# Optimization experiments

Hardware: AMD Instinct MI355X
Metric: run time of the kernel (lower is better)

Reference implementation:

```python
import jax, jax.numpy as jnp
import numpy as np
from jax import lax

NUM_CLASSES = 21
KSIZE = 11
DIL = 1
BLUR = 4
NUM_STEPS = 5
YX_SCALE = 80.0
RGB_SCALE = 13.0
POS_SCALE = 3.0


def _ceil_pad_factor(sizes, factor):
    offs = tuple((factor - s % factor) % factor for s in sizes)
    return tuple((o + 1) // 2 for o in offs)


def avg_pool_nopad(x, k, pad):
    # F.avg_pool2d(kernel=stride=k, padding=pad, count_include_pad=False)
    pcfg = ((0, 0), (0, 0), (pad[0], pad[0]), (pad[1], pad[1]))
    s = lax.reduce_window(x, jnp.float32(0), lax.add, (1, 1, k, k), (1, 1, k, k), pcfg)
    ones = jnp.ones((1, 1) + x.shape[2:], x.dtype)
    cnt = lax.reduce_window(ones, jnp.float32(0), lax.add, (1, 1, k, k), (1, 1, k, k), pcfg)
    return s / cnt


def _patches(x, k, dil):
    # im2col with zero padding (matches torch F.unfold used by pac)
    pad = (k // 2) * dil
    p = lax.conv_general_dilated_patches(
        x, (k, k), (1, 1), [(pad, pad), (pad, pad)], rhs_dilation=(dil, dil))
    B, C, H, W = x.shape
    return p.reshape(B, C, k * k, H, W)


def gaussian_kernel(feat, k, dil):
    # pixel-adaptive Gaussian kernel: exp(-0.5 * ||f_i - f_j||^2) over the KxK window
    p = _patches(feat, k, dil)                       # [B,F,k2,H,W]
    d = p - feat[:, :, None]
    return jnp.exp(-0.5 * jnp.sum(d * d, axis=1))    # [B,k2,H,W]


def pac_message(Q, kernel, k, dil):
    # shared-filter (Potts, spatial_filter=False) pac conv: per-channel kernel-weighted sum
    p = _patches(Q, k, dil)                          # [B,C,k2,h,w]
    return jnp.einsum('bckhw,bkhw->bchw', p, kernel)


def upsample_bilinear(x, scale):
    # matches F.interpolate(mode='bilinear', align_corners=False)
    B, C, h, w = x.shape
    def idx_w(n_in):
        n_out = n_in * scale
        src = jnp.clip((jnp.arange(n_out, dtype=jnp.float32) + 0.5) / scale - 0.5, 0.0, n_in - 1.0)
        i0 = jnp.floor(src).astype(jnp.int32)
        i1 = jnp.minimum(i0 + 1, n_in - 1)
        return i0, i1, (src - i0).astype(x.dtype)
    y0, y1, wy = idx_w(h)
    x0, x1, wx = idx_w(w)
    xh = x[:, :, y0, :] * (1 - wy)[None, None, :, None] + x[:, :, y1, :] * wy[None, None, :, None]
    return xh[:, :, :, x0] * (1 - wx)[None, None, None, :] + xh[:, :, :, x1] * wx[None, None, None, :]


def crf_forward(x, w_backbone, b_backbone, unary_weight, pairwise_weights):
    B, _, H, W = x.shape
    # backbone stub: 3x3 conv producing unary logits [B,21,H,W]
    unary = lax.conv_general_dilated(
        x, w_backbone, (1, 1), [(1, 1), (1, 1)],
        dimension_numbers=('NCHW', 'OIHW', 'NCHW')) + b_backbone[None, :, None, None]
    # edge features: bilateral (YX/80, RGB/13) and spatial (YX/3)
    yx = jnp.stack(jnp.meshgrid(jnp.arange(H, dtype=x.dtype), jnp.arange(W, dtype=x.dtype), indexing='ij'))
    yx = jnp.broadcast_to(yx[None], (B, 2, H, W))
    feat_bilateral = jnp.concatenate([yx / YX_SCALE, x / RGB_SCALE], axis=1)  # [B,5,H,W]
    feat_spatial = yx / POS_SCALE                                             # [B,2,H,W]
    pad = _ceil_pad_factor((H, W), BLUR)
    kernels = [gaussian_kernel(avg_pool_nopad(f, BLUR, pad), KSIZE, DIL)
               for f in (feat_bilateral, feat_spatial)]

    def step(logQ, unary, k1, k2, uw, pw):
        Q = jax.nn.softmax(logQ, axis=1)
        Qb = avg_pool_nopad(Q, BLUR, pad)
        new = uw * unary
        for kern, w in ((k1, pw[0]), (k2, pw[1])):
            msg = pac_message(Qb, kern, KSIZE, DIL)
            msg = upsample_bilinear(msg, BLUR)[:, :, pad[0]:pad[0] + H, pad[1]:pad[1] + W]
            new = new + w * msg
        return new

    logQ = unary
    for _ in range(NUM_STEPS):
        logQ = step(logQ, unary, kernels[0], kernels[1], unary_weight, pairwise_weights)
    return logQ  # final_output == 'log_Q'


def setup_inputs():
    key = jax.random.key(0)
    ks = jax.random.split(key, 3)
    B, H, W = 2, 512, 512
    x = jax.random.uniform(ks[0], (B, 3, H, W), jnp.float32) * 255.0  # image in [0,255]
    w_backbone = jax.random.normal(ks[1], (NUM_CLASSES, 3, 3, 3), jnp.float32) * 0.1
    b_backbone = jax.random.normal(ks[2], (NUM_CLASSES,), jnp.float32) * 0.01
    unary_weight = jnp.asarray(0.8, jnp.float32)
    pairwise_weights = jnp.asarray([2.0, 0.6], jnp.float32)
    return {"x": x, "w_backbone": w_backbone, "b_backbone": b_backbone,
            "unary_weight": unary_weight, "pairwise_weights": pairwise_weights}


def reference(x, w_backbone, b_backbone, unary_weight, pairwise_weights):
    return crf_forward(x, w_backbone, b_backbone, unary_weight, pairwise_weights)
```

## Files before the change

kernel.cpp:

```cpp
#include <hip/hip_runtime.h>

#define NCH 21
#define HWF (1 << 18)
#define HWP (1 << 14)
#define KS 11
#define KK 121
#define KPAD 5
#define TW 32
#define TH 8
#define HALO 5
#define LW (TW + 2 * HALO)
#define LH (TH + 2 * HALO)
#define LPLANE (LW * LH)

__global__ __launch_bounds__(256) void k_conv(const float* __restrict__ x,
                                              const float* __restrict__ w,
                                              const float* __restrict__ bias,
                                              float* __restrict__ unary) {
    int idx = blockIdx.x * 256 + threadIdx.x;
    int b = idx >> 16;
    int rem = idx & 65535;
    int y = rem >> 7;
    int xq = (rem & 127) << 2;

    float p[3][3][6];
#pragma unroll
    for (int ch = 0; ch < 3; ++ch) {
        const float* xp = x + (((size_t)(b * 3 + ch)) << 18);
#pragma unroll
        for (int r = 0; r < 3; ++r) {
            int yy = y + r - 1;
            if ((unsigned)yy >= 512u) {
#pragma unroll
                for (int j = 0; j < 6; ++j) p[ch][r][j] = 0.f;
            } else {
                const float* row = xp + (yy << 9);
                float4 v = *(const float4*)(row + xq);
                p[ch][r][1] = v.x; p[ch][r][2] = v.y; p[ch][r][3] = v.z; p[ch][r][4] = v.w;
                p[ch][r][0] = (xq > 0) ? row[xq - 1] : 0.f;
                p[ch][r][5] = (xq + 4 < 512) ? row[xq + 4] : 0.f;
            }
        }
    }
    for (int o = 0; o < NCH; ++o) {
        const float* wp = w + o * 27;
        float bz = bias[o];
        float a0 = bz, a1 = bz, a2 = bz, a3 = bz;
#pragma unroll
        for (int ch = 0; ch < 3; ++ch)
#pragma unroll
            for (int r = 0; r < 3; ++r) {
                float w0 = wp[ch * 9 + r * 3 + 0];
                float w1 = wp[ch * 9 + r * 3 + 1];
                float w2 = wp[ch * 9 + r * 3 + 2];
                const float* pr = p[ch][r];
                a0 += w0 * pr[0] + w1 * pr[1] + w2 * pr[2];
                a1 += w0 * pr[1] + w1 * pr[2] + w2 * pr[3];
                a2 += w0 * pr[2] + w1 * pr[3] + w2 * pr[4];
                a3 += w0 * pr[3] + w1 * pr[4] + w2 * pr[5];
            }
        float4 ov = make_float4(a0, a1, a2, a3);
        *(float4*)(unary + (((size_t)(b * NCH + o)) << 18) + (y << 9) + xq) = ov;
    }
}

__global__ __launch_bounds__(256) void k_pool_rgb(const float* __restrict__ x,
                                                  float* __restrict__ prgb) {
    int idx = blockIdx.x * 256 + threadIdx.x;
    int p = idx & (HWP - 1);
    int ch = (idx >> 14) % 3;
    int b = idx / (3 * HWP);
    int py = p >> 7, px = p & 127;
    const float* xp = x + (((size_t)(b * 3 + ch)) << 18);
    float s = 0.f;
#pragma unroll
    for (int r = 0; r < 4; ++r) {
        const float4 v = *(const float4*)(xp + (((4 * py + r) << 9) + 4 * px));
        s += v.x + v.y + v.z + v.w;
    }
    prgb[idx] = s * 0.0625f;
}

__global__ __launch_bounds__(256) void k_build_kc(const float* __restrict__ prgb,
                                                  const float* __restrict__ pw,
                                                  float* __restrict__ kc) {
    int idx = blockIdx.x * 256 + threadIdx.x;
    int p = idx & (HWP - 1);
    int jj = idx >> 14;
    int b = (jj >= KK) ? 1 : 0;
    int j = jj - KK * b;
    int dy = j / KS, dx = j - dy * KS;
    int py = p >> 7, px = p & 127;
    float pw0 = pw[0], pw1 = pw[1];

    const float inv13 = 1.0f / 13.0f;
    float fy = (4.f * py + 1.5f) * (1.0f / 80.0f);
    float fx = (4.f * px + 1.5f) * (1.0f / 80.0f);
    const float* pb = prgb + (size_t)b * 3 * HWP;
    float r0 = pb[p] * inv13;
    float g0 = pb[HWP + p] * inv13;
    float b0 = pb[2 * HWP + p] * inv13;
    float sy = (4.f * py + 1.5f) * (1.0f / 3.0f);
    float sx = (4.f * px + 1.5f) * (1.0f / 3.0f);

    int ny = py + dy - KPAD;
    int nx = px + dx - KPAD;
    float s1, s2;
    if ((unsigned)ny < 128u && (unsigned)nx < 128u) {
        int np = (ny << 7) + nx;
        float r2 = pb[np] * inv13;
        float g2 = pb[HWP + np] * inv13;
        float b2 = pb[2 * HWP + np] * inv13;
        float dya = fy - (4.f * ny + 1.5f) * (1.0f / 80.0f);
        float dxa = fx - (4.f * nx + 1.5f) * (1.0f / 80.0f);
        float dr = r0 - r2, dg = g0 - g2, db = b0 - b2;
        s1 = dya * dya + dxa * dxa + dr * dr + dg * dg + db * db;
        float dys = sy - (4.f * ny + 1.5f) * (1.0f / 3.0f);
        float dxs = sx - (4.f * nx + 1.5f) * (1.0f / 3.0f);
        s2 = dys * dys + dxs * dxs;
    } else {
        s1 = fy * fy + fx * fx + r0 * r0 + g0 * g0 + b0 * b0;
        s2 = sy * sy + sx * sx;
    }
    kc[idx] = pw0 * __expf(-0.5f * s1) + pw1 * __expf(-0.5f * s2);
}

__global__ __launch_bounds__(256) void k_softmax_pool(const float* __restrict__ logq,
                                                      float* __restrict__ qb) {
    int t = blockIdx.x * 256 + threadIdx.x;
    int sub = t & 15;
    int pp = t >> 4;
    int px = pp & 127, py = (pp >> 7) & 127, b = pp >> 14;
    int r = sub >> 2, i2 = sub & 3;
    int pix = ((4 * py + r) << 9) + 4 * px + i2;
    const float* sp = logq + (((size_t)(b * NCH)) << 18);

    float v[NCH];
#pragma unroll
    for (int c = 0; c < NCH; ++c) v[c] = sp[((size_t)c << 18) + pix];
    float m = v[0];
#pragma unroll
    for (int c = 1; c < NCH; ++c) m = fmaxf(m, v[c]);
    float s = 0.f;
#pragma unroll
    for (int c = 0; c < NCH; ++c) { v[c] = __expf(v[c] - m); s += v[c]; }
    float inv = 1.0f / s;
#pragma unroll
    for (int c = 0; c < NCH; ++c) {
        float q = v[c] * inv;
        q += __shfl_xor(q, 1, 16);
        q += __shfl_xor(q, 2, 16);
        q += __shfl_xor(q, 4, 16);
        q += __shfl_xor(q, 8, 16);
        if (sub == 0) qb[(((size_t)(b * NCH + c)) << 14) + (py << 7) + px] = q * 0.0625f;
    }
}

__global__ __launch_bounds__(256) void k_pac(const float* __restrict__ qb,
                                             const float* __restrict__ kc,
                                             float* __restrict__ msgc) {
    int tile = blockIdx.x & 63;
    int g = (blockIdx.x >> 6) & 3;
    int b = blockIdx.x >> 8;
    int c0 = g * 6;
    int ncg = (g == 3) ? 3 : 6;
    int tx0 = (tile & 3) * TW;
    int ty0 = (tile >> 2) * TH;

    __shared__ float lq[6 * LPLANE];

    const float* qbase = qb + (((size_t)(b * NCH + c0)) << 14);
    for (int i = threadIdx.x; i < 6 * LPLANE; i += 256) {
        int ch = i / LPLANE;
        int rem = i - ch * LPLANE;
        int ly = rem / LW, lx = rem - ly * LW;
        int gy = ty0 + ly - HALO, gx = tx0 + lx - HALO;
        float v = 0.f;
        if (ch < ncg && (unsigned)gy < 128u && (unsigned)gx < 128u)
            v = qbase[((size_t)ch << 14) + (gy << 7) + gx];
        lq[i] = v;
    }
    __syncthreads();

    int tx = threadIdx.x & 31, ty = threadIdx.x >> 5;
    int p = ((ty0 + ty) << 7) + (tx0 + tx);
    const float* kcb = kc + (((size_t)b * KK) << 14) + p;
    float a0 = 0.f, a1 = 0.f, a2 = 0.f, a3 = 0.f, a4 = 0.f, a5 = 0.f;
    for (int dy = 0; dy < KS; ++dy) {
        const float* lrow = lq + (ty + dy) * LW + tx;
        const float* kcrow = kcb + (((size_t)(dy * KS)) << 14);
#pragma unroll
        for (int dx = 0; dx < KS; ++dx) {
            float k = kcrow[((size_t)dx) << 14];
            const float* lp = lrow + dx;
            a0 += k * lp[0 * LPLANE];
            a1 += k * lp[1 * LPLANE];
            a2 += k * lp[2 * LPLANE];
            a3 += k * lp[3 * LPLANE];
            a4 += k * lp[4 * LPLANE];
            a5 += k * lp[5 * LPLANE];
        }
    }
    float* outp = msgc + (((size_t)(b * NCH + c0)) << 14) + p;
    outp[0] = a0;
    outp[(size_t)1 << 14] = a1;
    outp[(size_t)2 << 14] = a2;
    if (ncg == 6) {
        outp[(size_t)3 << 14] = a3;
        outp[(size_t)4 << 14] = a4;
        outp[(size_t)5 << 14] = a5;
    }
}

__global__ __launch_bounds__(256) void k_step(const float* __restrict__ unary,
                                              const float* __restrict__ msgc,
                                              const float* __restrict__ uwp,
                                              float* __restrict__ qb) {
    int t = blockIdx.x * 256 + threadIdx.x;
    int sub = t & 15;
    int pp = t >> 4;
    int px = pp & 127, py = (pp >> 7) & 127, b = pp >> 14;
    int r = sub >> 2, i2 = sub & 3;
    int y = 4 * py + r, x = 4 * px + i2;
    int pix = (y << 9) + x;
    float uw = uwp[0];

    float syf = fminf(fmaxf(y * 0.25f - 0.375f, 0.0f), 127.0f);
    int y0 = (int)syf; float fy = syf - y0; int y1 = min(y0 + 1, 127);
    float sxf = fminf(fmaxf(x * 0.25f - 0.375f, 0.0f), 127.0f);
    int x0 = (int)sxf; float fx = sxf - x0; int x1 = min(x0 + 1, 127);
    int o00 = (y0 << 7) + x0, o01 = (y0 << 7) + x1;
    int o10 = (y1 << 7) + x0, o11 = (y1 << 7) + x1;

    const float* up = unary + (((size_t)(b * NCH)) << 18) + pix;
    const float* mp = msgc + (((size_t)(b * NCH)) << 14);

    float v[NCH];
#pragma unroll
    for (int c = 0; c < NCH; ++c) {
        float v00 = mp[o00], v01 = mp[o01], v10 = mp[o10], v11 = mp[o11];
        float a = v00 + (v10 - v00) * fy;
        float bb = v01 + (v11 - v01) * fy;
        float val = a + (bb - a) * fx;
        v[c] = uw * up[(size_t)c << 18] + val;
        mp += HWP;
    }
    float m = v[0];
#pragma unroll
    for (int c = 1; c < NCH; ++c) m = fmaxf(m, v[c]);
    float ssum = 0.f;
#pragma unroll
    for (int c = 0; c < NCH; ++c) { v[c] = __expf(v[c] - m); ssum += v[c]; }
    float inv = 1.0f / ssum;
#pragma unroll
    for (int c = 0; c < NCH; ++c) {
        float qv = v[c] * inv;
        qv += __shfl_xor(qv, 1, 16);
        qv += __shfl_xor(qv, 2, 16);
        qv += __shfl_xor(qv, 4, 16);
        qv += __shfl_xor(qv, 8, 16);
        if (sub == 0) qb[(((size_t)(b * NCH + c)) << 14) + (py << 7) + px] = qv * 0.0625f;
    }
}

__global__ __launch_bounds__(256) void k_upcombine(const float* __restrict__ unary,
                                                   const float* __restrict__ msgc,
                                                   const float* __restrict__ uwp,
                                                   float* __restrict__ out) {
    int idx = blockIdx.x * 256 + threadIdx.x;
    float uw = uwp[0];
    int x = idx & 511, y = (idx >> 9) & 511;
    int t = idx >> 18;

    float syf = fminf(fmaxf(y * 0.25f - 0.375f, 0.0f), 127.0f);
    int y0 = (int)syf; float fy = syf - y0; int y1 = min(y0 + 1, 127);
    float sxf = fminf(fmaxf(x * 0.25f - 0.375f, 0.0f), 127.0f);
    int x0 = (int)sxf; float fx = sxf - x0; int x1 = min(x0 + 1, 127);

    const float* mp = msgc + (((size_t)t) << 14);
    float v00 = mp[(y0 << 7) + x0];
    float v01 = mp[(y0 << 7) + x1];
    float v10 = mp[(y1 << 7) + x0];
    float v11 = mp[(y1 << 7) + x1];
    float a = v00 + (v10 - v00) * fy;
    float bl = v01 + (v11 - v01) * fy;
    float val = a + (bl - a) * fx;

    out[idx] = uw * unary[idx] + val;
}

extern "C" void kernel_launch(void* const* d_in, const int* in_sizes, int n_in,
                              void* d_out, int out_size, void* d_ws, size_t ws_size,
                              hipStream_t stream) {
    const float* x  = (const float*)d_in[0];
    const float* wb = (const float*)d_in[1];
    const float* bb = (const float*)d_in[2];
    const float* uw = (const float*)d_in[3];
    const float* pw = (const float*)d_in[4];
    float* out = (float*)d_out;

    float* ws    = (float*)d_ws;
    float* unary = ws;
    float* kc    = unary + 11010048;
    float* qb    = kc + 3964928;
    float* msgc  = qb + 688128;
    float* prgb  = msgc;

    k_conv<<<512, 256, 0, stream>>>(x, wb, bb, unary);
    k_pool_rgb<<<384, 256, 0, stream>>>(x, prgb);
    k_build_kc<<<15488, 256, 0, stream>>>(prgb, pw, kc);
    k_softmax_pool<<<2048, 256, 0, stream>>>(unary, qb);

    for (int s = 0; s < 5; ++s) {
        k_pac<<<512, 256, 0, stream>>>(qb, kc, msgc);
        if (s < 4)
            k_step<<<2048, 256, 0, stream>>>(unary, msgc, uw, qb);
        else
            k_upcombine<<<43008, 256, 0, stream>>>(unary, msgc, uw, out);
    }
}
```

Baseline: 323.6 us.

## Fuse conv with softmax-pool, register-tile PAC, vectorize step with fixed bilinear weights

The first softmax-pool is folded into the backbone conv kernel, so the unary tensor is not re-read right after it is written. The PAC message kernel now loads all 21 channels into shared memory once per tile. Each thread computes a 4-pixel by 6-channel register tile from float4 row buffers and float4 kernel loads. The step kernel uses float4 unary access and precomputed fixed bilinear weights, and also takes over the final output combine through a flag. The trade-offs are fewer blocks for PAC (256 blocks of 128 threads) and heavy register use, which may lower occupancy.

```diff
diff --git a/kernel.cpp b/kernel.cpp
--- a/kernel.cpp
+++ b/kernel.cpp
@@ -1,47 +1,49 @@
 #include <hip/hip_runtime.h>
 
 #define NCH 21
-#define HWF (1 << 18)
 #define HWP (1 << 14)
 #define KS 11
 #define KK 121
-#define KPAD 5
-#define TW 32
-#define TH 8
-#define HALO 5
-#define LW (TW + 2 * HALO)
-#define LH (TH + 2 * HALO)
-#define LPLANE (LW * LH)
-
-__global__ __launch_bounds__(256) void k_conv(const float* __restrict__ x,
-                                              const float* __restrict__ w,
-                                              const float* __restrict__ bias,
-                                              float* __restrict__ unary) {
+#define PTW 16
+#define PTH 8
+#define LQW 28
+#define LQH 18
+#define LQPLANE (LQW * LQH)
+#define LQC 24
+
+__global__ __launch_bounds__(256) void k_conv_sm(const float* __restrict__ x,
+                                                 const float* __restrict__ w,
+                                                 const float* __restrict__ bias,
+                                                 float* __restrict__ unary,
+                                                 float* __restrict__ qb) {
     int idx = blockIdx.x * 256 + threadIdx.x;
+    int r = idx & 3;
+    int xqi = (idx >> 2) & 127;
+    int py = (idx >> 9) & 127;
     int b = idx >> 16;
-    int rem = idx & 65535;
-    int y = rem >> 7;
-    int xq = (rem & 127) << 2;
+    int y = 4 * py + r;
+    int xq = xqi << 2;
 
     float p[3][3][6];
 #pragma unroll
     for (int ch = 0; ch < 3; ++ch) {
         const float* xp = x + (((size_t)(b * 3 + ch)) << 18);
 #pragma unroll
-        for (int r = 0; r < 3; ++r) {
-            int yy = y + r - 1;
+        for (int rr = 0; rr < 3; ++rr) {
+            int yy = y + rr - 1;
             if ((unsigned)yy >= 512u) {
 #pragma unroll
-                for (int j = 0; j < 6; ++j) p[ch][r][j] = 0.f;
+                for (int j = 0; j < 6; ++j) p[ch][rr][j] = 0.f;
             } else {
                 const float* row = xp + (yy << 9);
                 float4 v = *(const float4*)(row + xq);
-                p[ch][r][1] = v.x; p[ch][r][2] = v.y; p[ch][r][3] = v.z; p[ch][r][4] = v.w;
-                p[ch][r][0] = (xq > 0) ? row[xq - 1] : 0.f;
-                p[ch][r][5] = (xq + 4 < 512) ? row[xq + 4] : 0.f;
+                p[ch][rr][1] = v.x; p[ch][rr][2] = v.y; p[ch][rr][3] = v.z; p[ch][rr][4] = v.w;
+                p[ch][rr][0] = (xq > 0) ? row[xq - 1] : 0.f;
+                p[ch][rr][5] = (xq + 4 < 512) ? row[xq + 4] : 0.f;
             }
         }
     }
+    float a[NCH][4];
     for (int o = 0; o < NCH; ++o) {
         const float* wp = w + o * 27;
         float bz = bias[o];
@@ -49,18 +51,41 @@
 #pragma unroll
         for (int ch = 0; ch < 3; ++ch)
 #pragma unroll
-            for (int r = 0; r < 3; ++r) {
-                float w0 = wp[ch * 9 + r * 3 + 0];
-                float w1 = wp[ch * 9 + r * 3 + 1];
-                float w2 = wp[ch * 9 + r * 3 + 2];
-                const float* pr = p[ch][r];
+            for (int rr = 0; rr < 3; ++rr) {
+                float w0 = wp[ch * 9 + rr * 3 + 0];
+                float w1 = wp[ch * 9 + rr * 3 + 1];
+                float w2 = wp[ch * 9 + rr * 3 + 2];
+                const float* pr = p[ch][rr];
                 a0 += w0 * pr[0] + w1 * pr[1] + w2 * pr[2];
                 a1 += w0 * pr[1] + w1 * pr[2] + w2 * pr[3];
                 a2 += w0 * pr[2] + w1 * pr[3] + w2 * pr[4];
                 a3 += w0 * pr[3] + w1 * pr[4] + w2 * pr[5];
             }
-        float4 ov = make_float4(a0, a1, a2, a3);
-        *(float4*)(unary + (((size_t)(b * NCH + o)) << 18) + (y << 9) + xq) = ov;
+        *(float4*)(unary + (((size_t)(b * NCH + o)) << 18) + (y << 9) + xq) =
+            make_float4(a0, a1, a2, a3);
+        a[o][0] = a0; a[o][1] = a1; a[o][2] = a2; a[o][3] = a3;
+    }
+    float qsum[NCH];
+#pragma unroll
+    for (int c = 0; c < NCH; ++c) qsum[c] = 0.f;
+#pragma unroll
+    for (int i2 = 0; i2 < 4; ++i2) {
+        float m = a[0][i2];
+#pragma unroll
+        for (int c = 1; c < NCH; ++c) m = fmaxf(m, a[c][i2]);
+        float s = 0.f;
+#pragma unroll
+        for (int c = 0; c < NCH; ++c) { float e = __expf(a[c][i2] - m); a[c][i2] = e; s += e; }
+        float inv = 1.0f / s;
+#pragma unroll
+        for (int c = 0; c < NCH; ++c) qsum[c] += a[c][i2] * inv;
+    }
+#pragma unroll
+    for (int c = 0; c < NCH; ++c) {
+        float v = qsum[c];
+        v += __shfl_xor(v, 1);
+        v += __shfl_xor(v, 2);
+        if (r == 0) qb[(((size_t)(b * NCH + c)) << 14) + (py << 7) + xqi] = v * 0.0625f;
     }
 }
 
@@ -103,8 +128,8 @@
     float sy = (4.f * py + 1.5f) * (1.0f / 3.0f);
     float sx = (4.f * px + 1.5f) * (1.0f / 3.0f);
 
-    int ny = py + dy - KPAD;
-    int nx = px + dx - KPAD;
+    int ny = py + dy - 5;
+    int nx = px + dx - 5;
     float s1, s2;
     if ((unsigned)ny < 128u && (unsigned)nx < 128u) {
         int np = (ny << 7) + nx;
@@ -125,168 +150,150 @@
     kc[idx] = pw0 * __expf(-0.5f * s1) + pw1 * __expf(-0.5f * s2);
 }
 
-__global__ __launch_bounds__(256) void k_softmax_pool(const float* __restrict__ logq,
-                                                      float* __restrict__ qb) {
-    int t = blockIdx.x * 256 + threadIdx.x;
-    int sub = t & 15;
-    int pp = t >> 4;
-    int px = pp & 127, py = (pp >> 7) & 127, b = pp >> 14;
-    int r = sub >> 2, i2 = sub & 3;
-    int pix = ((4 * py + r) << 9) + 4 * px + i2;
-    const float* sp = logq + (((size_t)(b * NCH)) << 18);
-
-    float v[NCH];
-#pragma unroll
-    for (int c = 0; c < NCH; ++c) v[c] = sp[((size_t)c << 18) + pix];
-    float m = v[0];
-#pragma unroll
-    for (int c = 1; c < NCH; ++c) m = fmaxf(m, v[c]);
-    float s = 0.f;
-#pragma unroll
-    for (int c = 0; c < NCH; ++c) { v[c] = __expf(v[c] - m); s += v[c]; }
-    float inv = 1.0f / s;
-#pragma unroll
-    for (int c = 0; c < NCH; ++c) {
-        float q = v[c] * inv;
-        q += __shfl_xor(q, 1, 16);
-        q += __shfl_xor(q, 2, 16);
-        q += __shfl_xor(q, 4, 16);
-        q += __shfl_xor(q, 8, 16);
-        if (sub == 0) qb[(((size_t)(b * NCH + c)) << 14) + (py << 7) + px] = q * 0.0625f;
-    }
-}
-
-__global__ __launch_bounds__(256) void k_pac(const float* __restrict__ qb,
-                                             const float* __restrict__ kc,
-                                             float* __restrict__ msgc) {
-    int tile = blockIdx.x & 63;
-    int g = (blockIdx.x >> 6) & 3;
-    int b = blockIdx.x >> 8;
+__global__ __launch_bounds__(128) void k_pac3(const float* __restrict__ qb,
+                                              const float* __restrict__ kc,
+                                              float* __restrict__ msgc) {
+    int tx0 = (blockIdx.x & 7) * PTW;
+    int ty0 = ((blockIdx.x >> 3) & 15) * PTH;
+    int b = blockIdx.x >> 7;
+
+    __shared__ float lq[LQC * LQPLANE];
+
+    const float* qbb = qb + (((size_t)(b * NCH)) << 14);
+    for (int i = threadIdx.x; i < LQC * LQPLANE; i += 128) {
+        int c = i / LQPLANE;
+        int rem = i - c * LQPLANE;
+        int ly = rem / LQW;
+        int lx = rem - ly * LQW;
+        int gy = ty0 + ly - 5, gx = tx0 + lx - 5;
+        float v = 0.f;
+        if (c < NCH && (unsigned)gy < 128u && (unsigned)gx < 128u)
+            v = qbb[((size_t)c << 14) + (gy << 7) + gx];
+        lq[i] = v;
+    }
+    __syncthreads();
+
+    int g = threadIdx.x >> 5;
+    int s = threadIdx.x & 31;
+    int my = s >> 2;
+    int mx0 = (s & 3) << 2;
     int c0 = g * 6;
-    int ncg = (g == 3) ? 3 : 6;
-    int tx0 = (tile & 3) * TW;
-    int ty0 = (tile >> 2) * TH;
-
-    __shared__ float lq[6 * LPLANE];
-
-    const float* qbase = qb + (((size_t)(b * NCH + c0)) << 14);
-    for (int i = threadIdx.x; i < 6 * LPLANE; i += 256) {
-        int ch = i / LPLANE;
-        int rem = i - ch * LPLANE;
-        int ly = rem / LW, lx = rem - ly * LW;
-        int gy = ty0 + ly - HALO, gx = tx0 + lx - HALO;
-        float v = 0.f;
-        if (ch < ncg && (unsigned)gy < 128u && (unsigned)gx < 128u)
-            v = qbase[((size_t)ch << 14) + (gy << 7) + gx];
-        lq[i] = v;
-    }
-    __syncthreads();
-
-    int tx = threadIdx.x & 31, ty = threadIdx.x >> 5;
-    int p = ((ty0 + ty) << 7) + (tx0 + tx);
-    const float* kcb = kc + (((size_t)b * KK) << 14) + p;
-    float a0 = 0.f, a1 = 0.f, a2 = 0.f, a3 = 0.f, a4 = 0.f, a5 = 0.f;
+
+    float acc[6][4];
+#pragma unroll
+    for (int c = 0; c < 6; ++c)
+#pragma unroll
+        for (int m = 0; m < 4; ++m) acc[c][m] = 0.f;
+
+    int p0 = ((ty0 + my) << 7) + tx0 + mx0;
+    const float* kcb = kc + (((size_t)(b * KK)) << 14) + p0;
+
     for (int dy = 0; dy < KS; ++dy) {
-        const float* lrow = lq + (ty + dy) * LW + tx;
-        const float* kcrow = kcb + (((size_t)(dy * KS)) << 14);
+        const float* lrow = lq + c0 * LQPLANE + (my + dy) * LQW + mx0;
+        float rb[6][16];
+#pragma unroll
+        for (int c = 0; c < 6; ++c) {
+            const float* lp = lrow + c * LQPLANE;
+            float4 v0 = *(const float4*)(lp + 0);
+            float4 v1 = *(const float4*)(lp + 4);
+            float4 v2 = *(const float4*)(lp + 8);
+            float4 v3 = *(const float4*)(lp + 12);
+            rb[c][0] = v0.x;  rb[c][1] = v0.y;  rb[c][2] = v0.z;  rb[c][3] = v0.w;
+            rb[c][4] = v1.x;  rb[c][5] = v1.y;  rb[c][6] = v1.z;  rb[c][7] = v1.w;
+            rb[c][8] = v2.x;  rb[c][9] = v2.y;  rb[c][10] = v2.z; rb[c][11] = v2.w;
+            rb[c][12] = v3.x; rb[c][13] = v3.y; rb[c][14] = v3.z; rb[c][15] = v3.w;
+        }
 #pragma unroll
         for (int dx = 0; dx < KS; ++dx) {
-            float k = kcrow[((size_t)dx) << 14];
-            const float* lp = lrow + dx;
-            a0 += k * lp[0 * LPLANE];
-            a1 += k * lp[1 * LPLANE];
-            a2 += k * lp[2 * LPLANE];
-            a3 += k * lp[3 * LPLANE];
-            a4 += k * lp[4 * LPLANE];
-            a5 += k * lp[5 * LPLANE];
+            float4 k4 = *(const float4*)(kcb + (((size_t)(dy * KS + dx)) << 14));
+#pragma unroll
+            for (int c = 0; c < 6; ++c) {
+                acc[c][0] += k4.x * rb[c][dx + 0];
+                acc[c][1] += k4.y * rb[c][dx + 1];
+                acc[c][2] += k4.z * rb[c][dx + 2];
+                acc[c][3] += k4.w * rb[c][dx + 3];
+            }
         }
     }
-    float* outp = msgc + (((size_t)(b * NCH + c0)) << 14) + p;
-    outp[0] = a0;
-    outp[(size_t)1 << 14] = a1;
-    outp[(size_t)2 << 14] = a2;
-    if (ncg == 6) {
-        outp[(size_t)3 << 14] = a3;
-        outp[(size_t)4 << 14] = a4;
-        outp[(size_t)5 << 14] = a5;
+#pragma unroll
+    for (int c = 0; c < 6; ++c) {
+        int ch = c0 + c;
+        if (ch < NCH)
+            *(float4*)(msgc + (((size_t)(b * NCH + ch)) << 14) + p0) =
+                make_float4(acc[c][0], acc[c][1], acc[c][2], acc[c][3]);
     }
 }
 
 __global__ __launch_bounds__(256) void k_step(const float* __restrict__ unary,
                                               const float* __restrict__ msgc,
                                               const float* __restrict__ uwp,
-                                              float* __restrict__ qb) {
-    int t = blockIdx.x * 256 + threadIdx.x;
-    int sub = t & 15;
-    int pp = t >> 4;
-    int px = pp & 127, py = (pp >> 7) & 127, b = pp >> 14;
-    int r = sub >> 2, i2 = sub & 3;
-    int y = 4 * py + r, x = 4 * px + i2;
-    int pix = (y << 9) + x;
+                                              float* __restrict__ qb,
+                                              float* __restrict__ out,
+                                              int write_out) {
+    int idx = blockIdx.x * 256 + threadIdx.x;
+    int r = idx & 3;
+    int px = (idx >> 2) & 127;
+    int py = (idx >> 9) & 127;
+    int b = idx >> 16;
+    int y = 4 * py + r;
     float uw = uwp[0];
 
-    float syf = fminf(fmaxf(y * 0.25f - 0.375f, 0.0f), 127.0f);
-    int y0 = (int)syf; float fy = syf - y0; int y1 = min(y0 + 1, 127);
-    float sxf = fminf(fmaxf(x * 0.25f - 0.375f, 0.0f), 127.0f);
-    int x0 = (int)sxf; float fx = sxf - x0; int x1 = min(x0 + 1, 127);
-    int o00 = (y0 << 7) + x0, o01 = (y0 << 7) + x1;
-    int o10 = (y1 << 7) + x0, o11 = (y1 << 7) + x1;
-
-    const float* up = unary + (((size_t)(b * NCH)) << 18) + pix;
+    int rA = (r < 2) ? max(py - 1, 0) : py;
+    int rB = (r < 2) ? py : min(py + 1, 127);
+    float fy = (r == 0) ? 0.625f : (r == 1) ? 0.875f : (r == 2) ? 0.125f : 0.375f;
+    int xm1 = max(px - 1, 0), xp1 = min(px + 1, 127);
+    int oA = rA << 7, oB = rB << 7;
+
+    size_t base = (((size_t)(b * NCH)) << 18) + (y << 9) + (px << 2);
+    const float* up = unary + base;
     const float* mp = msgc + (((size_t)(b * NCH)) << 14);
 
-    float v[NCH];
+    float a[NCH][4];
 #pragma unroll
     for (int c = 0; c < NCH; ++c) {
-        float v00 = mp[o00], v01 = mp[o01], v10 = mp[o10], v11 = mp[o11];
-        float a = v00 + (v10 - v00) * fy;
-        float bb = v01 + (v11 - v01) * fy;
-        float val = a + (bb - a) * fx;
-        v[c] = uw * up[(size_t)c << 18] + val;
-        mp += HWP;
-    }
-    float m = v[0];
-#pragma unroll
-    for (int c = 1; c < NCH; ++c) m = fmaxf(m, v[c]);
-    float ssum = 0.f;
-#pragma unroll
-    for (int c = 0; c < NCH; ++c) { v[c] = __expf(v[c] - m); ssum += v[c]; }
-    float inv = 1.0f / ssum;
+        float4 u4 = *(const float4*)(up + ((size_t)c << 18));
+        const float* m0 = mp + ((size_t)c << 14);
+        float aL = m0[oA + xm1], aM = m0[oA + px], aR = m0[oA + xp1];
+        float bL = m0[oB + xm1], bM = m0[oB + px], bR = m0[oB + xp1];
+        float cL = aL + (bL - aL) * fy;
+        float cM = aM + (bM - aM) * fy;
+        float cR = aR + (bR - aR) * fy;
+        a[c][0] = uw * u4.x + cL + (cM - cL) * 0.625f;
+        a[c][1] = uw * u4.y + cL + (cM - cL) * 0.875f;
+        a[c][2] = uw * u4.z + cM + (cR - cM) * 0.125f;
+        a[c][3] = uw * u4.w + cM + (cR - cM) * 0.375f;
+    }
+
+    if (write_out) {
+        float* op = out + base;
+#pragma unroll
+        for (int c = 0; c < NCH; ++c)
+            *(float4*)(op + ((size_t)c << 18)) = make_float4(a[c][0], a[c][1], a[c][2], a[c][3]);
+        return;
+    }
+
+    float qsum[NCH];
+#pragma unroll
+    for (int c = 0; c < NCH; ++c) qsum[c] = 0.f;
+#pragma unroll
+    for (int i2 = 0; i2 < 4; ++i2) {
+        float m = a[0][i2];
+#pragma unroll
+        for (int c = 1; c < NCH; ++c) m = fmaxf(m, a[c][i2]);
+        float ss = 0.f;
+#pragma unroll
+        for (int c = 0; c < NCH; ++c) { float e = __expf(a[c][i2] - m); a[c][i2] = e; ss += e; }
+        float inv = 1.0f / ss;
+#pragma unroll
+        for (int c = 0; c < NCH; ++c) qsum[c] += a[c][i2] * inv;
+    }
 #pragma unroll
     for (int c = 0; c < NCH; ++c) {
-        float qv = v[c] * inv;
-        qv += __shfl_xor(qv, 1, 16);
-        qv += __shfl_xor(qv, 2, 16);
-        qv += __shfl_xor(qv, 4, 16);
-        qv += __shfl_xor(qv, 8, 16);
-        if (sub == 0) qb[(((size_t)(b * NCH + c)) << 14) + (py << 7) + px] = qv * 0.0625f;
-    }
-}
-
-__global__ __launch_bounds__(256) void k_upcombine(const float* __restrict__ unary,
-                                                   const float* __restrict__ msgc,
-                                                   const float* __restrict__ uwp,
-                                                   float* __restrict__ out) {
-    int idx = blockIdx.x * 256 + threadIdx.x;
-    float uw = uwp[0];
-    int x = idx & 511, y = (idx >> 9) & 511;
-    int t = idx >> 18;
-
-    float syf = fminf(fmaxf(y * 0.25f - 0.375f, 0.0f), 127.0f);
-    int y0 = (int)syf; float fy = syf - y0; int y1 = min(y0 + 1, 127);
-    float sxf = fminf(fmaxf(x * 0.25f - 0.375f, 0.0f), 127.0f);
-    int x0 = (int)sxf; float fx = sxf - x0; int x1 = min(x0 + 1, 127);
-
-    const float* mp = msgc + (((size_t)t) << 14);
-    float v00 = mp[(y0 << 7) + x0];
-    float v01 = mp[(y0 << 7) + x1];
-    float v10 = mp[(y1 << 7) + x0];
-    float v11 = mp[(y1 << 7) + x1];
-    float a = v00 + (v10 - v00) * fy;
-    float bl = v01 + (v11 - v01) * fy;
-    float val = a + (bl - a) * fx;
-
-    out[idx] = uw * unary[idx] + val;
+        float v = qsum[c];
+        v += __shfl_xor(v, 1);
+        v += __shfl_xor(v, 2);
+        if (r == 0) qb[(((size_t)(b * NCH + c)) << 14) + (py << 7) + px] = v * 0.0625f;
+    }
 }
 
 extern "C" void kernel_launch(void* const* d_in, const int* in_sizes, int n_in,
@@ -306,16 +313,12 @@
     float* msgc  = qb + 688128;
     float* prgb  = msgc;
 
-    k_conv<<<512, 256, 0, stream>>>(x, wb, bb, unary);
+    k_conv_sm<<<512, 256, 0, stream>>>(x, wb, bb, unary, qb);
     k_pool_rgb<<<384, 256, 0, stream>>>(x, prgb);
     k_build_kc<<<15488, 256, 0, stream>>>(prgb, pw, kc);
-    k_softmax_pool<<<2048, 256, 0, stream>>>(unary, qb);
 
     for (int s = 0; s < 5; ++s) {
-        k_pac<<<512, 256, 0, stream>>>(qb, kc, msgc);
-        if (s < 4)
-            k_step<<<2048, 256, 0, stream>>>(unary, msgc, uw, qb);
-        else
-            k_upcombine<<<43008, 256, 0, stream>>>(unary, msgc, uw, out);
-    }
-}
+        k_pac3<<<256, 128, 0, stream>>>(qb, kc, msgc);
+        k_step<<<512, 256, 0, stream>>>(unary, msgc, uw, qb, out, (s == 4) ? 1 : 0);
+    }
+}
```

Result: slower. 400.6 us (+23.8%).
